# Performance work log

Hardware: AMD Instinct MI355X
Metric: run time of the kernel (lower is better)

Reference implementation:

```python
import jax, jax.numpy as jnp
import numpy as np

B, CIN, HIN, WIN = 2, 64, 128, 256
COUT, K = 64, 3
STRIDE, PAD, DIL = 1, 1, 1
HOUT = (HIN + 2 * PAD - DIL * (K - 1) - 1) // STRIDE + 1
WOUT = (WIN + 2 * PAD - DIL * (K - 1) - 1) // STRIDE + 1
KK = K * K


def setup_inputs() -> dict:
    key = jax.random.key(0)
    k1, k2, k3, k4 = jax.random.split(key, 4)
    x = jax.random.normal(k1, (B, CIN, HIN, WIN), jnp.float32)
    # precomputed geometric offsets (cached in the original module); interleaved (y, x) per kernel tap
    offset = jax.random.normal(k2, (B, 2 * KK, HOUT, WOUT), jnp.float32)
    fan_in = CIN * K * K
    weight = jax.random.normal(k3, (COUT, CIN, K, K), jnp.float32) / np.float32(np.sqrt(fan_in))
    bias = jax.random.uniform(k4, (COUT,), jnp.float32, -1.0, 1.0) / np.float32(np.sqrt(fan_in))
    return {"x": x, "offset": offset, "weight": weight, "bias": bias}


def _deform_conv2d(x, offset, weight, bias):
    Bn, Cin, Hin, Win = x.shape
    Cout, _, Kh, Kw = weight.shape
    _, _, Ho, Wo = offset.shape
    kk = Kh * Kw
    off = offset.reshape(Bn, kk, 2, Ho, Wo)
    off_y, off_x = off[:, :, 0], off[:, :, 1]  # [B, KK, Ho, Wo]

    ki, kj = jnp.meshgrid(jnp.arange(Kh), jnp.arange(Kw), indexing='ij')
    # base sampling grid: output pos * stride - pad + kernel tap * dilation
    base_y = (jnp.arange(Ho) * STRIDE - PAD)[None, :, None] + (ki.reshape(-1) * DIL)[:, None, None]
    base_x = (jnp.arange(Wo) * STRIDE - PAD)[None, None, :] + (kj.reshape(-1) * DIL)[:, None, None]
    py = base_y[None].astype(x.dtype) + off_y  # [B, KK, Ho, Wo]
    px = base_x[None].astype(x.dtype) + off_x

    y0f = jnp.floor(py)
    x0f = jnp.floor(px)
    wy = py - y0f  # bilinear weights
    wx = px - x0f
    y0 = y0f.astype(jnp.int32)
    x0 = x0f.astype(jnp.int32)

    x_flat = x.reshape(Bn, Cin, Hin * Win)

    def corner(yi, xi):
        valid = ((yi >= 0) & (yi < Hin) & (xi >= 0) & (xi < Win)).astype(x.dtype)
        idx = jnp.clip(yi, 0, Hin - 1) * Win + jnp.clip(xi, 0, Win - 1)  # [B, KK, Ho, Wo]

        def gather_one(img, idx_b):
            return jnp.take(img, idx_b.reshape(-1), axis=1).reshape(Cin, kk, Ho, Wo)

        vals = jax.vmap(gather_one)(x_flat, idx)  # [B, Cin, KK, Ho, Wo]
        return vals * valid[:, None]

    one = jnp.asarray(1.0, x.dtype)
    sampled = (corner(y0, x0) * ((one - wy) * (one - wx))[:, None]
               + corner(y0, x0 + 1) * ((one - wy) * wx)[:, None]
               + corner(y0 + 1, x0) * (wy * (one - wx))[:, None]
               + corner(y0 + 1, x0 + 1) * (wy * wx)[:, None])  # [B, Cin, KK, Ho, Wo]

    w = weight.reshape(Cout, Cin, kk)
    out = jnp.einsum('bckhw,ock->bohw', sampled, w) + bias[None, :, None, None]
    return out


def reference(x, offset, weight, bias):
    return _deform_conv2d(x, offset, weight, bias)
```

## Files before the change

kernel.cpp:

```cpp
#include <hip/hip_runtime.h>
#include <hip/hip_bf16.h>


constexpr int CI = 64, HI = 128, WI = 256;
constexpr int CO = 64, KK = 9, HO = 128, WO = 256;
constexpr int HWi = HI * WI;
constexpr int HWo = HO * WO;

typedef __attribute__((ext_vector_type(4))) float f32x4;
typedef __attribute__((ext_vector_type(8))) short s16x8;
typedef __attribute__((ext_vector_type(4))) unsigned int u32x4;

__device__ __forceinline__ short to_bf16(float f) {
    __hip_bfloat16 h = __float2bfloat16(f);
    return *reinterpret_cast<short*>(&h);
}
__device__ __forceinline__ float bf2f(short s) {
    unsigned int u = ((unsigned int)(unsigned short)s) << 16;
    return __uint_as_float(u);
}

__global__ __launch_bounds__(256, 2) void xpose(
    const float* __restrict__ x, short* __restrict__ xt)
{
    __shared__ short st[256 * 66];
    const int tid = threadIdx.x;
    const int px0 = blockIdx.x * 256;
    const int b = px0 >> 15;
    const float* xb = x + (size_t)b * CI * HWi + (px0 & (HWi - 1));
    #pragma unroll 8
    for (int c = 0; c < CI; ++c)
        st[tid * 66 + c] = to_bf16(xb[(size_t)c * HWi + tid]);
    __syncthreads();
    const unsigned int* st32 = (const unsigned int*)st;
    #pragma unroll
    for (int r = 0; r < 4; ++r) {
        const int p = r * 64 + (tid >> 2), g = tid & 3;
        unsigned int v[8];
        #pragma unroll
        for (int j = 0; j < 8; ++j) v[j] = st32[p * 33 + g * 8 + j];
        unsigned int* dst = (unsigned int*)(xt + (size_t)(px0 + p) * 64 + g * 16);
        *(u32x4*)dst = u32x4{v[0], v[1], v[2], v[3]};
        *(u32x4*)(dst + 4) = u32x4{v[4], v[5], v[6], v[7]};
    }
}

__global__ void wpack_k(const float* __restrict__ w, short* __restrict__ wp)
{
    const int e = blockIdx.x * 256 + threadIdx.x;
    if (e >= KK * CO * CI) return;
    const int k = e >> 12, rem = e & 4095;
    wp[e] = to_bf16(w[(size_t)rem * KK + k]);
}

__global__ __launch_bounds__(256, 4) void dconv_mfma(
    const short* __restrict__ xt, const float* __restrict__ off,
    const short* __restrict__ wp, const float* __restrict__ bias,
    float* __restrict__ out)
{
    __shared__ short sS[64 * 64];
    __shared__ float pw[4][KK * 64];
    __shared__ int   pidx[4][KK * 64];

    const int tid = threadIdx.x, lane = tid & 63, wv = tid >> 6;
    const int wg = ((blockIdx.x & 7) << 7) | (blockIdx.x >> 3);
    const int b = wg >> 9, hot = (wg >> 4) & 31, wot = wg & 15;
    const int ho0 = hot * 4, wo0 = wot * 16;

    const float* offb = off + (size_t)b * (2 * KK * HWo);
    for (int e = tid; e < KK * 64; e += 256) {
        const int k = e >> 6, n = e & 63;
        const int ho = ho0 + (n >> 4), wo = wo0 + (n & 15);
        const int ki = k / 3, kj = k - 3 * ki;
        const float oy = offb[(2 * k) * HWo + ho * WO + wo];
        const float ox = offb[(2 * k + 1) * HWo + ho * WO + wo];
        const float py  = (float)(ho - 1 + ki) + oy;
        const float pxx = (float)(wo - 1 + kj) + ox;
        const float y0f = floorf(py), x0f = floorf(pxx);
        const float wy = py - y0f, wx = pxx - x0f;
        const int y0 = (int)y0f, x0 = (int)x0f;
        const int y1 = y0 + 1, x1 = x0 + 1;
        const float vy0 = (y0 >= 0 && y0 < HI) ? 1.f : 0.f;
        const float vy1 = (y1 >= 0 && y1 < HI) ? 1.f : 0.f;
        const float vx0 = (x0 >= 0 && x0 < WI) ? 1.f : 0.f;
        const float vx1 = (x1 >= 0 && x1 < WI) ? 1.f : 0.f;
        const int cy0 = min(max(y0, 0), HI - 1), cy1 = min(max(y1, 0), HI - 1);
        const int cx0 = min(max(x0, 0), WI - 1), cx1 = min(max(x1, 0), WI - 1);
        pw[0][e] = (1.f - wy) * (1.f - wx) * vy0 * vx0;
        pw[1][e] = (1.f - wy) * wx         * vy0 * vx1;
        pw[2][e] = wy         * (1.f - wx) * vy1 * vx0;
        pw[3][e] = wy         * wx         * vy1 * vx1;
        pidx[0][e] = (cy0 * WI + cx0) * 128;
        pidx[1][e] = (cy0 * WI + cx1) * 128;
        pidx[2][e] = (cy1 * WI + cx0) * 128;
        pidx[3][e] = (cy1 * WI + cx1) * 128;
    }

    f32x4 acc[4];
    {
        const int r0 = 16 * wv + 4 * (lane >> 4);
        const f32x4 ini = *(const f32x4*)(bias + r0);
        #pragma unroll
        for (int f = 0; f < 4; ++f) acc[f] = ini;
    }
    __syncthreads();

    const char* xtb = (const char*)xt + (size_t)b * HWi * 128;
    const int px = tid >> 2, cg = tid & 3, cb = cg * 32;
    const int mrow = 16 * wv + (lane & 15);
    const int ke = 8 * (lane >> 4);
    const int koffb = 16 * (lane >> 4);
    const int xr = (lane & 7) << 4;

    for (int k = 0; k < KK; ++k) {
        if (k) __syncthreads();

        const short* wpk = wp + k * 4096;
        const s16x8 a0 = *(const s16x8*)(wpk + mrow * 64 + ke);
        const s16x8 a1 = *(const s16x8*)(wpk + mrow * 64 + 32 + ke);

        float a[16];
        #pragma unroll
        for (int j = 0; j < 16; ++j) a[j] = 0.f;
        #pragma unroll
        for (int c4 = 0; c4 < 4; ++c4) {
            const float wc = pw[c4][k * 64 + px];
            const int ofs = pidx[c4][k * 64 + px];
            const s16x8 u0 = *(const s16x8*)(xtb + ofs + cb);
            const s16x8 u1 = *(const s16x8*)(xtb + ofs + cb + 16);
            #pragma unroll
            for (int j = 0; j < 8; ++j) {
                a[j]     = fmaf(wc, bf2f(u0[j]), a[j]);
                a[8 + j] = fmaf(wc, bf2f(u1[j]), a[8 + j]);
            }
        }
        s16x8 v0, v1;
        #pragma unroll
        for (int j = 0; j < 8; ++j) { v0[j] = to_bf16(a[j]); v1[j] = to_bf16(a[8 + j]); }
        *(s16x8*)((char*)sS + ((px * 128 + cb) ^ ((px & 7) << 4))) = v0;
        *(s16x8*)((char*)sS + ((px * 128 + cb + 16) ^ ((px & 7) << 4))) = v1;
        __syncthreads();

        #pragma unroll
        for (int f = 0; f < 4; ++f) {
            const int nrow = 16 * f + (lane & 15);
            const s16x8 b0 = *(const s16x8*)((const char*)sS + ((nrow * 128 + koffb) ^ xr));
            const s16x8 b1 = *(const s16x8*)((const char*)sS + ((nrow * 128 + 64 + koffb) ^ xr));
            acc[f] = __builtin_amdgcn_mfma_f32_16x16x32_bf16(a0, b0, acc[f], 0, 0, 0);
            acc[f] = __builtin_amdgcn_mfma_f32_16x16x32_bf16(a1, b1, acc[f], 0, 0, 0);
        }
    }

    #pragma unroll
    for (int f = 0; f < 4; ++f) {
        const int ho = ho0 + f;
        const int wo = wo0 + (lane & 15);
        const int m0 = 16 * wv + 4 * (lane >> 4);
        float* po = out + (((size_t)(b * CO + m0) * HO + ho) * WO + wo);
        #pragma unroll
        for (int r = 0; r < 4; ++r)
            po[(size_t)r * HWo] = acc[f][r];
    }
}

extern "C" void kernel_launch(void* const* d_in, const int* in_sizes, int n_in,
                              void* d_out, int out_size, void* d_ws, size_t ws_size,
                              hipStream_t stream) {
    const float* x    = (const float*)d_in[0];
    const float* off  = (const float*)d_in[1];
    const float* wgt  = (const float*)d_in[2];
    const float* bias = (const float*)d_in[3];
    float* out = (float*)d_out;
    short* xt = (short*)d_ws;
    short* wp = (short*)((char*)d_ws + (size_t)2 * HWi * 64 * 2);
    xpose<<<dim3(256), dim3(256), 0, stream>>>(x, xt);
    wpack_k<<<dim3(144), dim3(256), 0, stream>>>(wgt, wp);
    dconv_mfma<<<dim3(1024), dim3(256), 0, stream>>>(xt, off, wp, bias, out);
}
```

Measured before the change: 103.1 us.

## Double-buffer shared sample tile and prefetch next tap's gathers and weights

Makes the shared sampled tile double-buffered, removing one barrier per kernel tap. The four bilinear corner gathers and the weight fragments for the next tap are issued before the barrier and MFMA of the current tap, so their global latency overlaps with compute. This adds 16 live VGPRs for the prefetched gathers plus extra LDS, which may reduce occupancy under the 4-blocks launch bound.

```diff
diff --git a/kernel.cpp b/kernel.cpp
--- a/kernel.cpp
+++ b/kernel.cpp
@@ -58,7 +58,7 @@
     const short* __restrict__ wp, const float* __restrict__ bias,
     float* __restrict__ out)
 {
-    __shared__ short sS[64 * 64];
+    __shared__ short sS[2][64 * 64];
     __shared__ float pw[4][KK * 64];
     __shared__ int   pidx[4][KK * 64];
 
@@ -111,44 +111,65 @@
     const int ke = 8 * (lane >> 4);
     const int koffb = 16 * (lane >> 4);
     const int xr = (lane & 7) << 4;
-
+    const int swz0 = (px * 128 + cb) ^ ((px & 7) << 4);
+    const int swz1 = (px * 128 + cb + 16) ^ ((px & 7) << 4);
+
+    s16x8 u[8], a0, a1;
+    #pragma unroll
+    for (int c4 = 0; c4 < 4; ++c4) {
+        const int ofs = pidx[c4][px];
+        u[2 * c4]     = *(const s16x8*)(xtb + ofs + cb);
+        u[2 * c4 + 1] = *(const s16x8*)(xtb + ofs + cb + 16);
+    }
+    a0 = *(const s16x8*)(wp + mrow * 64 + ke);
+    a1 = *(const s16x8*)(wp + mrow * 64 + 32 + ke);
+
+    int p = 0;
     for (int k = 0; k < KK; ++k) {
-        if (k) __syncthreads();
-
-        const short* wpk = wp + k * 4096;
-        const s16x8 a0 = *(const s16x8*)(wpk + mrow * 64 + ke);
-        const s16x8 a1 = *(const s16x8*)(wpk + mrow * 64 + 32 + ke);
-
-        float a[16];
-        #pragma unroll
-        for (int j = 0; j < 16; ++j) a[j] = 0.f;
+        float s[16];
+        #pragma unroll
+        for (int j = 0; j < 16; ++j) s[j] = 0.f;
         #pragma unroll
         for (int c4 = 0; c4 < 4; ++c4) {
             const float wc = pw[c4][k * 64 + px];
-            const int ofs = pidx[c4][k * 64 + px];
-            const s16x8 u0 = *(const s16x8*)(xtb + ofs + cb);
-            const s16x8 u1 = *(const s16x8*)(xtb + ofs + cb + 16);
             #pragma unroll
             for (int j = 0; j < 8; ++j) {
-                a[j]     = fmaf(wc, bf2f(u0[j]), a[j]);
-                a[8 + j] = fmaf(wc, bf2f(u1[j]), a[8 + j]);
+                s[j]     = fmaf(wc, bf2f(u[2 * c4][j]), s[j]);
+                s[8 + j] = fmaf(wc, bf2f(u[2 * c4 + 1][j]), s[8 + j]);
             }
         }
         s16x8 v0, v1;
         #pragma unroll
-        for (int j = 0; j < 8; ++j) { v0[j] = to_bf16(a[j]); v1[j] = to_bf16(a[8 + j]); }
-        *(s16x8*)((char*)sS + ((px * 128 + cb) ^ ((px & 7) << 4))) = v0;
-        *(s16x8*)((char*)sS + ((px * 128 + cb + 16) ^ ((px & 7) << 4))) = v1;
+        for (int j = 0; j < 8; ++j) { v0[j] = to_bf16(s[j]); v1[j] = to_bf16(s[8 + j]); }
+        char* sp = (char*)sS[p];
+        *(s16x8*)(sp + swz0) = v0;
+        *(s16x8*)(sp + swz1) = v1;
+
+        if (k + 1 < KK) {
+            #pragma unroll
+            for (int c4 = 0; c4 < 4; ++c4) {
+                const int ofs = pidx[c4][(k + 1) * 64 + px];
+                u[2 * c4]     = *(const s16x8*)(xtb + ofs + cb);
+                u[2 * c4 + 1] = *(const s16x8*)(xtb + ofs + cb + 16);
+            }
+        }
         __syncthreads();
 
+        const char* spc = (const char*)sS[p];
         #pragma unroll
         for (int f = 0; f < 4; ++f) {
             const int nrow = 16 * f + (lane & 15);
-            const s16x8 b0 = *(const s16x8*)((const char*)sS + ((nrow * 128 + koffb) ^ xr));
-            const s16x8 b1 = *(const s16x8*)((const char*)sS + ((nrow * 128 + 64 + koffb) ^ xr));
+            const s16x8 b0 = *(const s16x8*)(spc + ((nrow * 128 + koffb) ^ xr));
+            const s16x8 b1 = *(const s16x8*)(spc + ((nrow * 128 + 64 + koffb) ^ xr));
             acc[f] = __builtin_amdgcn_mfma_f32_16x16x32_bf16(a0, b0, acc[f], 0, 0, 0);
             acc[f] = __builtin_amdgcn_mfma_f32_16x16x32_bf16(a1, b1, acc[f], 0, 0, 0);
         }
+        if (k + 1 < KK) {
+            const short* wpk1 = wp + (k + 1) * 4096;
+            a0 = *(const s16x8*)(wpk1 + mrow * 64 + ke);
+            a1 = *(const s16x8*)(wpk1 + mrow * 64 + 32 + ke);
+        }
+        p ^= 1;
     }
 
     #pragma unroll
```

Result: faster. 100.8 us (-2.2%).

## Halve conv tile to 32 pixels, double-buffer shared tile, fuse weight pack

Applied to the files above, without the earlier changes.

The weight-packing kernel is folded into the transpose kernel, which removes one launch. The deform-conv kernel now processes 32 output pixels per block instead of 64, with 2048 blocks and launch bounds raised to 8 blocks per CU. Each thread gathers 4 corners of 8 channels at once, and the sampled tile is double-buffered so one barrier per tap is dropped. The intent is higher occupancy and more gather latency in flight. In exchange, the per-block offset and weight-fragment loads are amortised over fewer pixels.

```diff
diff --git a/kernel.cpp b/kernel.cpp
--- a/kernel.cpp
+++ b/kernel.cpp
@@ -6,6 +6,7 @@
 constexpr int CO = 64, KK = 9, HO = 128, WO = 256;
 constexpr int HWi = HI * WI;
 constexpr int HWo = HO * WO;
+constexpr int NPX = 32;
 
 typedef __attribute__((ext_vector_type(4))) float f32x4;
 typedef __attribute__((ext_vector_type(8))) short s16x8;
@@ -21,7 +22,8 @@
 }
 
 __global__ __launch_bounds__(256, 2) void xpose(
-    const float* __restrict__ x, short* __restrict__ xt)
+    const float* __restrict__ x, short* __restrict__ xt,
+    const float* __restrict__ w, short* __restrict__ wp)
 {
     __shared__ short st[256 * 66];
     const int tid = threadIdx.x;
@@ -31,6 +33,11 @@
     #pragma unroll 8
     for (int c = 0; c < CI; ++c)
         st[tid * 66 + c] = to_bf16(xb[(size_t)c * HWi + tid]);
+    if (blockIdx.x < 144) {
+        const int e = blockIdx.x * 256 + tid;
+        const int k = e >> 12, rem = e & 4095;
+        wp[e] = to_bf16(w[(size_t)rem * KK + k]);
+    }
     __syncthreads();
     const unsigned int* st32 = (const unsigned int*)st;
     #pragma unroll
@@ -45,31 +52,23 @@
     }
 }
 
-__global__ void wpack_k(const float* __restrict__ w, short* __restrict__ wp)
-{
-    const int e = blockIdx.x * 256 + threadIdx.x;
-    if (e >= KK * CO * CI) return;
-    const int k = e >> 12, rem = e & 4095;
-    wp[e] = to_bf16(w[(size_t)rem * KK + k]);
-}
-
-__global__ __launch_bounds__(256, 4) void dconv_mfma(
+__global__ __launch_bounds__(256, 8) void dconv_mfma(
     const short* __restrict__ xt, const float* __restrict__ off,
     const short* __restrict__ wp, const float* __restrict__ bias,
     float* __restrict__ out)
 {
-    __shared__ short sS[64 * 64];
-    __shared__ float pw[4][KK * 64];
-    __shared__ int   pidx[4][KK * 64];
+    __shared__ short sS[2][NPX * 64];
+    __shared__ float pw[4][KK * NPX];
+    __shared__ int   pidx[4][KK * NPX];
 
     const int tid = threadIdx.x, lane = tid & 63, wv = tid >> 6;
-    const int wg = ((blockIdx.x & 7) << 7) | (blockIdx.x >> 3);
-    const int b = wg >> 9, hot = (wg >> 4) & 31, wot = wg & 15;
-    const int ho0 = hot * 4, wo0 = wot * 16;
+    const int wg = ((blockIdx.x & 7) << 8) | (blockIdx.x >> 3);
+    const int b = wg >> 10, hot = (wg >> 4) & 63, wot = wg & 15;
+    const int ho0 = hot * 2, wo0 = wot * 16;
 
     const float* offb = off + (size_t)b * (2 * KK * HWo);
-    for (int e = tid; e < KK * 64; e += 256) {
-        const int k = e >> 6, n = e & 63;
+    for (int e = tid; e < KK * NPX; e += 256) {
+        const int k = e >> 5, n = e & 31;
         const int ho = ho0 + (n >> 4), wo = wo0 + (n & 15);
         const int ki = k / 3, kj = k - 3 * ki;
         const float oy = offb[(2 * k) * HWo + ho * WO + wo];
@@ -96,63 +95,60 @@
         pidx[3][e] = (cy1 * WI + cx1) * 128;
     }
 
-    f32x4 acc[4];
+    f32x4 acc[2];
     {
         const int r0 = 16 * wv + 4 * (lane >> 4);
         const f32x4 ini = *(const f32x4*)(bias + r0);
-        #pragma unroll
-        for (int f = 0; f < 4; ++f) acc[f] = ini;
+        acc[0] = ini; acc[1] = ini;
     }
     __syncthreads();
 
     const char* xtb = (const char*)xt + (size_t)b * HWi * 128;
-    const int px = tid >> 2, cg = tid & 3, cb = cg * 32;
+    const int px = tid >> 3, cb = (tid & 7) * 16;
     const int mrow = 16 * wv + (lane & 15);
     const int ke = 8 * (lane >> 4);
     const int koffb = 16 * (lane >> 4);
     const int xr = (lane & 7) << 4;
+    const int swz = (px * 128 + cb) ^ ((px & 7) << 4);
 
+    int p = 0;
     for (int k = 0; k < KK; ++k) {
-        if (k) __syncthreads();
+        const int e = k * NPX + px;
+        const s16x8 u0 = *(const s16x8*)(xtb + pidx[0][e] + cb);
+        const s16x8 u1 = *(const s16x8*)(xtb + pidx[1][e] + cb);
+        const s16x8 u2 = *(const s16x8*)(xtb + pidx[2][e] + cb);
+        const s16x8 u3 = *(const s16x8*)(xtb + pidx[3][e] + cb);
+        const float w0 = pw[0][e], w1 = pw[1][e], w2 = pw[2][e], w3 = pw[3][e];
+        s16x8 v;
+        #pragma unroll
+        for (int j = 0; j < 8; ++j) {
+            float s = w0 * bf2f(u0[j]);
+            s = fmaf(w1, bf2f(u1[j]), s);
+            s = fmaf(w2, bf2f(u2[j]), s);
+            s = fmaf(w3, bf2f(u3[j]), s);
+            v[j] = to_bf16(s);
+        }
+        *(s16x8*)((char*)sS[p] + swz) = v;
 
         const short* wpk = wp + k * 4096;
         const s16x8 a0 = *(const s16x8*)(wpk + mrow * 64 + ke);
         const s16x8 a1 = *(const s16x8*)(wpk + mrow * 64 + 32 + ke);
-
-        float a[16];
-        #pragma unroll
-        for (int j = 0; j < 16; ++j) a[j] = 0.f;
-        #pragma unroll
-        for (int c4 = 0; c4 < 4; ++c4) {
-            const float wc = pw[c4][k * 64 + px];
-            const int ofs = pidx[c4][k * 64 + px];
-            const s16x8 u0 = *(const s16x8*)(xtb + ofs + cb);
-            const s16x8 u1 = *(const s16x8*)(xtb + ofs + cb + 16);
-            #pragma unroll
-            for (int j = 0; j < 8; ++j) {
-                a[j]     = fmaf(wc, bf2f(u0[j]), a[j]);
-                a[8 + j] = fmaf(wc, bf2f(u1[j]), a[8 + j]);
-            }
-        }
-        s16x8 v0, v1;
-        #pragma unroll
-        for (int j = 0; j < 8; ++j) { v0[j] = to_bf16(a[j]); v1[j] = to_bf16(a[8 + j]); }
-        *(s16x8*)((char*)sS + ((px * 128 + cb) ^ ((px & 7) << 4))) = v0;
-        *(s16x8*)((char*)sS + ((px * 128 + cb + 16) ^ ((px & 7) << 4))) = v1;
         __syncthreads();
 
+        const char* spc = (const char*)sS[p];
         #pragma unroll
-        for (int f = 0; f < 4; ++f) {
+        for (int f = 0; f < 2; ++f) {
             const int nrow = 16 * f + (lane & 15);
-            const s16x8 b0 = *(const s16x8*)((const char*)sS + ((nrow * 128 + koffb) ^ xr));
-            const s16x8 b1 = *(const s16x8*)((const char*)sS + ((nrow * 128 + 64 + koffb) ^ xr));
+            const s16x8 b0 = *(const s16x8*)(spc + ((nrow * 128 + koffb) ^ xr));
+            const s16x8 b1 = *(const s16x8*)(spc + ((nrow * 128 + 64 + koffb) ^ xr));
             acc[f] = __builtin_amdgcn_mfma_f32_16x16x32_bf16(a0, b0, acc[f], 0, 0, 0);
             acc[f] = __builtin_amdgcn_mfma_f32_16x16x32_bf16(a1, b1, acc[f], 0, 0, 0);
         }
+        p ^= 1;
     }
 
     #pragma unroll
-    for (int f = 0; f < 4; ++f) {
+    for (int f = 0; f < 2; ++f) {
         const int ho = ho0 + f;
         const int wo = wo0 + (lane & 15);
         const int m0 = 16 * wv + 4 * (lane >> 4);
@@ -173,7 +169,6 @@
     float* out = (float*)d_out;
     short* xt = (short*)d_ws;
     short* wp = (short*)((char*)d_ws + (size_t)2 * HWi * 64 * 2);
-    xpose<<<dim3(256), dim3(256), 0, stream>>>(x, xt);
-    wpack_k<<<dim3(144), dim3(256), 0, stream>>>(wgt, wp);
-    dconv_mfma<<<dim3(1024), dim3(256), 0, stream>>>(xt, off, wp, bias, out);
+    xpose<<<dim3(256), dim3(256), 0, stream>>>(x, xt, wgt, wp);
+    dconv_mfma<<<dim3(2048), dim3(256), 0, stream>>>(xt, off, wp, bias, out);
 }
```

Result: slower. 107.0 us (+3.7%).
